# Kernel optimization log

Hardware: AMD Instinct MI355X
Metric: run time of the kernel (lower is better)

The kernel has to match this reference:

```python
import jax, jax.numpy as jnp
import numpy as np

EPS = 1e-5  # torch LayerNorm default


def _score_branch(feat, g, b, W1, B1, W2, B2):
    # feat: [B, C, H, W] -> tokens [B, H*W, C]
    B, C, H, Wd = feat.shape
    tokens = jnp.transpose(feat, (0, 2, 3, 1)).reshape(B, H * Wd, C)
    mu = tokens.mean(-1, keepdims=True)
    var = jnp.mean(jnp.square(tokens - mu), axis=-1, keepdims=True)
    x = (tokens - mu) * jax.lax.rsqrt(var + EPS) * g + b
    h = jax.nn.gelu(jnp.einsum('btc,cd->btd', x, W1) + B1, approximate=False)
    s = jax.nn.sigmoid(jnp.einsum('btd,do->bto', h, W2) + B2)  # [B, HW, 1]
    return s.reshape(B, 1, H, Wd)


def setup_inputs() -> dict:
    key = jax.random.key(0)
    ks = jax.random.split(key, 6)
    M, B, C, H, W = 3, 16, 768, 48, 48
    Ch = C // 4
    return {
        'feat0': jax.random.normal(ks[0], (B, C, H, W), jnp.float32),
        'feat1': jax.random.normal(ks[1], (B, C, H, W), jnp.float32),
        'feat2': jax.random.normal(ks[2], (B, C, H, W), jnp.float32),
        'ln_g': jnp.ones((M, C), jnp.float32),
        'ln_b': jnp.zeros((M, C), jnp.float32),
        'w1': jax.random.normal(ks[3], (M, C, Ch), jnp.float32) * 0.02,
        'b1': jnp.zeros((M, Ch), jnp.float32),
        'w2': jax.random.normal(ks[4], (M, Ch, 1), jnp.float32) * 0.02,
        'b2': jnp.zeros((M, 1), jnp.float32),
    }


def reference(feat0, feat1, feat2, ln_g, ln_b, w1, b1, w2, b2):
    feats = (feat0, feat1, feat2)
    outs = []
    for i, feat in enumerate(feats):  # fixed small loop over modalities
        outs.append(_score_branch(feat, ln_g[i], ln_b[i], w1[i], b1[i], w2[i], b2[i]))
    return tuple(outs)
```

## Files before the change

### kernel.cpp

```cpp
#include <hip/hip_runtime.h>
#include <hip/hip_bf16.h>

typedef __attribute__((ext_vector_type(8))) short bf16x8;
typedef __attribute__((ext_vector_type(4))) short bf16x4;
typedef __attribute__((ext_vector_type(4))) float f32x4;
typedef __attribute__((address_space(1))) const unsigned int gu32;
typedef __attribute__((address_space(3))) unsigned int lu32;

__device__ __forceinline__ unsigned short f2bf(float f) {
    __hip_bfloat16 h = __float2bfloat16(f);
    return __builtin_bit_cast(unsigned short, h);
}

template<int N> __device__ __forceinline__ void waitv() {
    asm volatile("s_waitcnt vmcnt(%0)" :: "i"(N) : "memory");
}
__device__ __forceinline__ void waitlgkm0() {
    asm volatile("s_waitcnt lgkmcnt(0)" ::: "memory");
}

#define BT 64
#define TPM 576
#define NCHUNK 24
#define DEPTH 4

__global__ void prep_partial(const float* __restrict__ w1, const float* __restrict__ lng,
                             const float* __restrict__ lnb,
                             float* __restrict__ upart, float* __restrict__ vpart)
{
    const int m   = blockIdx.x >> 3;
    const int seg = blockIdx.x & 7;
    const int d   = threadIdx.x;
    const float* w1m = w1 + (size_t)m * 768 * 192;
    const float* gm  = lng + m * 768;
    const float* bm  = lnb + m * 768;
    const int c0 = seg * 96;
    float su = 0.f, sv = 0.f;
    for (int c = 0; c < 96; ++c) {
        float wv = w1m[(size_t)(c0 + c) * 192 + d];
        su += gm[c0 + c] * wv;
        sv += bm[c0 + c] * wv;
    }
    upart[(m * 8 + seg) * 192 + d] = su;
    vpart[(m * 8 + seg) * 192 + d] = sv;
}

__global__ void prep_combine(const float* __restrict__ upart, const float* __restrict__ vpart,
                             const float* __restrict__ b1,
                             float* __restrict__ u, float* __restrict__ vb)
{
    const int m = blockIdx.x;
    const int d = threadIdx.x;
    float su = 0.f, sv = 0.f;
    for (int s = 0; s < 8; ++s) {
        su += upart[(m * 8 + s) * 192 + d];
        sv += vpart[(m * 8 + s) * 192 + d];
    }
    u[m * 192 + d]  = su;
    vb[m * 192 + d] = sv + b1[m * 192 + d];
}

__global__ void prep_pack(const float* __restrict__ w1, const float* __restrict__ lng,
                          unsigned short* __restrict__ w1f)
{
    const int m  = blockIdx.x / 24;
    const int kk = blockIdx.x % 24;
    const int tid = threadIdx.x;
    __shared__ float ws[32 * 192];
    const float* w1m = w1 + ((size_t)m * 768 + kk * 32) * 192;
    const float* gm  = lng + m * 768 + kk * 32;
    for (int i = tid; i < 6144; i += 256) {
        int cl = i / 192, d = i % 192;
        ws[i] = gm[cl] * w1m[(size_t)cl * 192 + d];
    }
    __syncthreads();
    unsigned short* outp = w1f + ((size_t)m * 24 + kk) * 6144;
    for (int i = tid; i < 6144; i += 256) {
        int nf   = i >> 9;
        int rem  = i & 511;
        int lane = rem >> 3;
        int j    = rem & 7;
        int cl   = ((lane >> 4) << 3) + j;
        int d    = (nf << 4) + (lane & 15);
        outp[i]  = f2bf(ws[cl * 192 + d]);
    }
}

__global__ __launch_bounds__(256, 3)
void fused_main(const float* __restrict__ f0, const float* __restrict__ f1,
                const float* __restrict__ f2,
                const unsigned short* __restrict__ w1f,
                const float* __restrict__ u_g, const float* __restrict__ vb_g,
                const float* __restrict__ w2_g, const float* __restrict__ b2_g,
                float* __restrict__ out)
{
    const int bx   = blockIdx.x;
    const int mod  = bx / TPM;
    const int tile = bx % TPM;
    const float* feat = (mod == 0) ? f0 : ((mod == 1) ? f1 : f2);
    const int T0   = tile * BT;
    const int bimg = T0 / 2304;
    const int hw0  = T0 % 2304;
    const float* fbase = feat + (size_t)bimg * 768 * 2304 + hw0;

    const int tid = threadIdx.x;
    const int l   = tid & 63;
    const int w   = tid >> 6;
    const int p   = l & 31;
    const int cg  = l >> 5;
    const int col = l & 15, lg = l >> 4;

    __shared__ float Fstage[DEPTH][32][64];
    __shared__ unsigned short Atile[64][40];
    __shared__ float redS[4][64], redQ[4][64];
    __shared__ float mu_s[64], rs_s[64];
    __shared__ float red2[4][64];

    const unsigned short* w1fm = w1f + (size_t)mod * 24 * 6144;

    f32x4 acc[4][3];
    #pragma unroll
    for (int a = 0; a < 4; ++a)
        #pragma unroll
        for (int b = 0; b < 3; ++b) acc[a][b] = (f32x4){0.f, 0.f, 0.f, 0.f};

    float sum0 = 0.f, ssq0 = 0.f, sum1 = 0.f, ssq1 = 0.f;
    bf16x8 bf[3];

    auto STAGE = [&](int src_kk, int qb) {
        #pragma unroll
        for (int j = 0; j < 2; ++j) {
            const float* src = fbase + (size_t)(src_kk * 32 + w * 8 + j * 4 + lg) * 2304
                                     + 4 * (l & 15);
            __builtin_amdgcn_global_load_lds((gu32*)src,
                                             (lu32*)&Fstage[qb][w * 8 + j * 4][0],
                                             16, 0, 0);
        }
    };
    auto LOADB = [&](int kk) {
        const bf16x8* sB = reinterpret_cast<const bf16x8*>(w1fm + (size_t)kk * 6144);
        #pragma unroll
        for (int nf = 0; nf < 3; ++nf)
            bf[nf] = sB[(w * 3 + nf) * 64 + l];
    };
    auto TOPB = [&]() {
        __builtin_amdgcn_sched_barrier(0);
        __builtin_amdgcn_s_barrier();
        __builtin_amdgcn_sched_barrier(0);
    };

    auto STEPR = [&](int kk, int qb) {
        const int t0 = 2 * p, t1 = t0 + 1;
        const int s0 = w ^ (((t0 >> 2) ^ (t0 >> 4)) & 3);
        const int s1 = w ^ (((t1 >> 2) ^ (t1 >> 4)) & 3);
        bf16x4 q0, q1;
        #pragma unroll
        for (int j = 0; j < 4; ++j) {
            float2 v = *reinterpret_cast<const float2*>(&Fstage[qb][w * 8 + cg * 4 + j][t0]);
            q0[j] = (short)f2bf(v.x);
            q1[j] = (short)f2bf(v.y);
            sum0 += v.x; ssq0 += v.x * v.x;
            sum1 += v.y; ssq1 += v.y * v.y;
        }
        *reinterpret_cast<bf16x4*>(&Atile[t0][s0 * 8 + cg * 4]) = q0;
        *reinterpret_cast<bf16x4*>(&Atile[t1][s1 * 8 + cg * 4]) = q1;
        waitlgkm0();
        TOPB();
        int kn = kk + DEPTH; if (kn > NCHUNK - 1) kn = NCHUNK - 1;
        STAGE(kn, qb);
        __builtin_amdgcn_sched_barrier(0);
        bf16x8 af[4];
        #pragma unroll
        for (int mf = 0; mf < 4; ++mf) {
            int t = mf * 16 + col;
            int s = lg ^ (((t >> 2) ^ (t >> 4)) & 3);
            af[mf] = *reinterpret_cast<const bf16x8*>(&Atile[t][s * 8]);
        }
        #pragma unroll
        for (int mf = 0; mf < 4; ++mf)
            #pragma unroll
            for (int nf = 0; nf < 3; ++nf)
                acc[mf][nf] = __builtin_amdgcn_mfma_f32_16x16x32_bf16(
                                  af[mf], bf[nf], acc[mf][nf], 0, 0, 0);
        int kb = kk + 1; if (kb > NCHUNK - 1) kb = NCHUNK - 1;
        LOADB(kb);
    };

    STAGE(0, 0); STAGE(1, 1); STAGE(2, 2); STAGE(3, 3);
    __builtin_amdgcn_sched_barrier(0);
    LOADB(0);
    __builtin_amdgcn_sched_barrier(0);

    waitv<9>();  TOPB(); STEPR(0, 0);
    waitv<12>(); TOPB(); STEPR(1, 1);
    waitv<15>(); TOPB(); STEPR(2, 2);
    #pragma unroll 1
    for (int kk = 3; kk < NCHUNK; ++kk) {
        waitv<18>(); TOPB(); STEPR(kk, kk & 3);
    }

    sum0 += __shfl_xor(sum0, 32);  sum1 += __shfl_xor(sum1, 32);
    ssq0 += __shfl_xor(ssq0, 32);  ssq1 += __shfl_xor(ssq1, 32);
    if (l < 32) {
        redS[w][2 * p] = sum0;  redS[w][2 * p + 1] = sum1;
        redQ[w][2 * p] = ssq0;  redQ[w][2 * p + 1] = ssq1;
    }
    __syncthreads();
    if (tid < 64) {
        float S = redS[0][tid] + redS[1][tid] + redS[2][tid] + redS[3][tid];
        float Q = redQ[0][tid] + redQ[1][tid] + redQ[2][tid] + redQ[3][tid];
        float mu = S * (1.f / 768.f);
        float var = Q * (1.f / 768.f) - mu * mu;
        mu_s[tid] = mu;
        rs_s[tid] = rsqrtf(var + 1e-5f);
    }
    __syncthreads();

    const float* um  = u_g  + mod * 192;
    const float* vbm = vb_g + mod * 192;
    const float* w2m = w2_g + mod * 192;
    float uf[3], vbf[3], w2f[3];
    #pragma unroll
    for (int nf = 0; nf < 3; ++nf) {
        int d = (w * 3 + nf) * 16 + col;
        uf[nf] = um[d]; vbf[nf] = vbm[d]; w2f[nf] = w2m[d];
    }
    float ps[4][4];
    #pragma unroll
    for (int mf = 0; mf < 4; ++mf) {
        #pragma unroll
        for (int r = 0; r < 4; ++r) {
            int t = mf * 16 + lg * 4 + r;
            float mu = mu_s[t], rs = rs_s[t];
            float pp = 0.f;
            #pragma unroll
            for (int nf = 0; nf < 3; ++nf) {
                float x = rs * (acc[mf][nf][r] - mu * uf[nf]) + vbf[nf];
                float h = 0.5f * x * (1.f + erff(x * 0.70710678118f));
                pp += h * w2f[nf];
            }
            ps[mf][r] = pp;
        }
    }
    #pragma unroll
    for (int m = 1; m < 16; m <<= 1)
        #pragma unroll
        for (int mf = 0; mf < 4; ++mf)
            #pragma unroll
            for (int r = 0; r < 4; ++r)
                ps[mf][r] += __shfl_xor(ps[mf][r], m, 64);
    if (col == 0) {
        #pragma unroll
        for (int mf = 0; mf < 4; ++mf)
            #pragma unroll
            for (int r = 0; r < 4; ++r)
                red2[w][mf * 16 + lg * 4 + r] = ps[mf][r];
    }
    __syncthreads();
    if (tid < 64) {
        float logit = red2[0][tid] + red2[1][tid] + red2[2][tid] + red2[3][tid] + b2_g[mod];
        out[(size_t)mod * 36864 + T0 + tid] = 1.f / (1.f + expf(-logit));
    }
}

extern "C" void kernel_launch(void* const* d_in, const int* in_sizes, int n_in,
                              void* d_out, int out_size, void* d_ws, size_t ws_size,
                              hipStream_t stream)
{
    const float* f0  = (const float*)d_in[0];
    const float* f1  = (const float*)d_in[1];
    const float* f2  = (const float*)d_in[2];
    const float* lng = (const float*)d_in[3];
    const float* lnb = (const float*)d_in[4];
    const float* w1  = (const float*)d_in[5];
    const float* b1  = (const float*)d_in[6];
    const float* w2  = (const float*)d_in[7];
    const float* b2  = (const float*)d_in[8];
    float* out = (float*)d_out;

    char* ws = (char*)d_ws;
    unsigned short* w1f = (unsigned short*)ws;
    float* u     = (float*)(ws + 884736);
    float* vb    = (float*)(ws + 887040);
    float* upart = (float*)(ws + 889344);
    float* vpart = (float*)(ws + 907776);

    prep_partial<<<dim3(24), dim3(192), 0, stream>>>(w1, lng, lnb, upart, vpart);
    prep_combine<<<dim3(3),  dim3(192), 0, stream>>>(upart, vpart, b1, u, vb);
    prep_pack   <<<dim3(72), dim3(256), 0, stream>>>(w1, lng, w1f);
    fused_main  <<<dim3(3 * TPM), dim3(256), 0, stream>>>(f0, f1, f2, w1f, u, vb, w2, b2, out);
}
```

Baseline: 122.4 us.

## Double-buffer A tile, triple-buffer B fragments, fully unroll K loop with one barrier per step

Restructures the main GEMM pipeline. Atile is double-buffered, so each step now needs one workgroup barrier instead of two. B-weight fragments are prefetched three chunks ahead into a rotating register set rather than one. The 24-chunk loop is fully unrolled with per-step vmcnt waits, and redundant clamped prefetches at the tail are dropped. This aims to cut barrier stalls and hide global load latency, at the cost of more registers and more code size.

After: 134.4 us. 9.8% more time.

```diff
diff --git a/kernel.cpp b/kernel.cpp
--- a/kernel.cpp
+++ b/kernel.cpp
@@ -18,11 +18,15 @@
 __device__ __forceinline__ void waitlgkm0() {
     asm volatile("s_waitcnt lgkmcnt(0)" ::: "memory");
 }
+__device__ __forceinline__ void sbar() {
+    __builtin_amdgcn_sched_barrier(0);
+    __builtin_amdgcn_s_barrier();
+    __builtin_amdgcn_sched_barrier(0);
+}
 
 #define BT 64
 #define TPM 576
 #define NCHUNK 24
-#define DEPTH 4
 
 __global__ void prep_partial(const float* __restrict__ w1, const float* __restrict__ lng,
                              const float* __restrict__ lnb,
@@ -110,8 +114,8 @@
     const int cg  = l >> 5;
     const int col = l & 15, lg = l >> 4;
 
-    __shared__ float Fstage[DEPTH][32][64];
-    __shared__ unsigned short Atile[64][40];
+    __shared__ float Fstage[4][32][64];
+    __shared__ unsigned short Atile[2][64][40];
     __shared__ float redS[4][64], redQ[4][64];
     __shared__ float mu_s[64], rs_s[64];
     __shared__ float red2[4][64];
@@ -125,7 +129,7 @@
         for (int b = 0; b < 3; ++b) acc[a][b] = (f32x4){0.f, 0.f, 0.f, 0.f};
 
     float sum0 = 0.f, ssq0 = 0.f, sum1 = 0.f, ssq1 = 0.f;
-    bf16x8 bf[3];
+    bf16x8 bf[3][3];
 
     auto STAGE = [&](int src_kk, int qb) {
         #pragma unroll
@@ -136,68 +140,74 @@
                                              (lu32*)&Fstage[qb][w * 8 + j * 4][0],
                                              16, 0, 0);
         }
-    };
-    auto LOADB = [&](int kk) {
-        const bf16x8* sB = reinterpret_cast<const bf16x8*>(w1fm + (size_t)kk * 6144);
-        #pragma unroll
-        for (int nf = 0; nf < 3; ++nf)
-            bf[nf] = sB[(w * 3 + nf) * 64 + l];
-    };
-    auto TOPB = [&]() {
-        __builtin_amdgcn_sched_barrier(0);
-        __builtin_amdgcn_s_barrier();
         __builtin_amdgcn_sched_barrier(0);
     };
-
-    auto STEPR = [&](int kk, int qb) {
-        const int t0 = 2 * p, t1 = t0 + 1;
-        const int s0 = w ^ (((t0 >> 2) ^ (t0 >> 4)) & 3);
-        const int s1 = w ^ (((t1 >> 2) ^ (t1 >> 4)) & 3);
-        bf16x4 q0, q1;
-        #pragma unroll
-        for (int j = 0; j < 4; ++j) {
-            float2 v = *reinterpret_cast<const float2*>(&Fstage[qb][w * 8 + cg * 4 + j][t0]);
-            q0[j] = (short)f2bf(v.x);
-            q1[j] = (short)f2bf(v.y);
-            sum0 += v.x; ssq0 += v.x * v.x;
-            sum1 += v.y; ssq1 += v.y * v.y;
-        }
-        *reinterpret_cast<bf16x4*>(&Atile[t0][s0 * 8 + cg * 4]) = q0;
-        *reinterpret_cast<bf16x4*>(&Atile[t1][s1 * 8 + cg * 4]) = q1;
-        waitlgkm0();
-        TOPB();
-        int kn = kk + DEPTH; if (kn > NCHUNK - 1) kn = NCHUNK - 1;
-        STAGE(kn, qb);
+    auto LOADB = [&](int kk, int bb) {
+        const bf16x8* sB = reinterpret_cast<const bf16x8*>(w1fm + (size_t)kk * 6144);
+        #pragma unroll
+        for (int nf = 0; nf < 3; ++nf)
+            bf[bb][nf] = sB[(w * 3 + nf) * 64 + l];
         __builtin_amdgcn_sched_barrier(0);
-        bf16x8 af[4];
-        #pragma unroll
-        for (int mf = 0; mf < 4; ++mf) {
-            int t = mf * 16 + col;
-            int s = lg ^ (((t >> 2) ^ (t >> 4)) & 3);
-            af[mf] = *reinterpret_cast<const bf16x8*>(&Atile[t][s * 8]);
-        }
-        #pragma unroll
-        for (int mf = 0; mf < 4; ++mf)
-            #pragma unroll
-            for (int nf = 0; nf < 3; ++nf)
-                acc[mf][nf] = __builtin_amdgcn_mfma_f32_16x16x32_bf16(
-                                  af[mf], bf[nf], acc[mf][nf], 0, 0, 0);
-        int kb = kk + 1; if (kb > NCHUNK - 1) kb = NCHUNK - 1;
-        LOADB(kb);
     };
 
-    STAGE(0, 0); STAGE(1, 1); STAGE(2, 2); STAGE(3, 3);
-    __builtin_amdgcn_sched_barrier(0);
-    LOADB(0);
-    __builtin_amdgcn_sched_barrier(0);
-
-    waitv<9>();  TOPB(); STEPR(0, 0);
-    waitv<12>(); TOPB(); STEPR(1, 1);
-    waitv<15>(); TOPB(); STEPR(2, 2);
-    #pragma unroll 1
-    for (int kk = 3; kk < NCHUNK; ++kk) {
-        waitv<18>(); TOPB(); STEPR(kk, kk & 3);
-    }
+#define STEPX(K, WN, DO_S, DO_B)                                               \
+    {                                                                          \
+        waitv<WN>();                                                           \
+        __builtin_amdgcn_sched_barrier(0);                                     \
+                   \
+        const int t0 = 2 * p, t1 = t0 + 1;                                     \
+        const int s0 = w ^ (((t0 >> 2) ^ (t0 >> 4)) & 3);                      \
+        const int s1 = w ^ (((t1 >> 2) ^ (t1 >> 4)) & 3);                      \
+        bf16x4 q0, q1;                                                         \
+        _Pragma("unroll")                                                      \
+        for (int j = 0; j < 4; ++j) {                                          \
+            float2 v = *reinterpret_cast<const float2*>(                       \
+                &Fstage[(K) & 3][w * 8 + cg * 4 + j][t0]);                     \
+            q0[j] = (short)f2bf(v.x);                                          \
+            q1[j] = (short)f2bf(v.y);                                          \
+            sum0 += v.x; ssq0 += v.x * v.x;                                    \
+            sum1 += v.y; ssq1 += v.y * v.y;                                    \
+        }                                                                      \
+        *reinterpret_cast<bf16x4*>(&Atile[(K) & 1][t0][s0 * 8 + cg * 4]) = q0; \
+        *reinterpret_cast<bf16x4*>(&Atile[(K) & 1][t1][s1 * 8 + cg * 4]) = q1; \
+        waitlgkm0();                                                           \
+        __builtin_amdgcn_sched_barrier(0);                                     \
+        if (DO_S) STAGE((K) + 4, (K) & 3);                                     \
+        sbar();                                                                \
+                                               \
+        bf16x8 af[4];                                                          \
+        _Pragma("unroll")                                                      \
+        for (int mf = 0; mf < 4; ++mf) {                                       \
+            int t = mf * 16 + col;                                             \
+            int s = lg ^ (((t >> 2) ^ (t >> 4)) & 3);                          \
+            af[mf] = *reinterpret_cast<const bf16x8*>(&Atile[(K) & 1][t][s * 8]); \
+        }                                                                      \
+        _Pragma("unroll")                                                      \
+        for (int mf = 0; mf < 4; ++mf)                                         \
+            _Pragma("unroll")                                                  \
+            for (int nf = 0; nf < 3; ++nf)                                     \
+                acc[mf][nf] = __builtin_amdgcn_mfma_f32_16x16x32_bf16(         \
+                                  af[mf], bf[(K) % 3][nf], acc[mf][nf], 0, 0, 0); \
+        if (DO_B) LOADB((K) + 3, (K) % 3);                                     \
+    }
+
+    STAGE(0, 0); LOADB(0, 0);
+    STAGE(1, 1); LOADB(1, 1);
+    STAGE(2, 2); LOADB(2, 2);
+    STAGE(3, 3);
+
+    STEPX(0, 15, true, true)   STEPX(1, 15, true, true)   STEPX(2, 15, true, true)
+    STEPX(3, 15, true, true)   STEPX(4, 18, true, true)   STEPX(5, 18, true, true)
+    STEPX(6, 18, true, true)   STEPX(7, 18, true, true)   STEPX(8, 18, true, true)
+    STEPX(9, 18, true, true)   STEPX(10, 18, true, true)  STEPX(11, 18, true, true)
+    STEPX(12, 18, true, true)  STEPX(13, 18, true, true)  STEPX(14, 18, true, true)
+    STEPX(15, 18, true, true)  STEPX(16, 18, true, true)  STEPX(17, 18, true, true)
+    STEPX(18, 18, true, true)  STEPX(19, 18, true, true)
+    STEPX(20, 18, false, true)
+    STEPX(21, 16, false, false)
+    STEPX(22, 11, false, false)
+    STEPX(23, 6,  false, false)
+#undef STEPX
 
     sum0 += __shfl_xor(sum0, 32);  sum1 += __shfl_xor(sum1, 32);
     ssq0 += __shfl_xor(ssq0, 32);  ssq1 += __shfl_xor(ssq1, 32);
```
